# Kernel optimization log

Hardware: AMD Instinct MI355X
Metric: run time of the kernel (lower is better)

Reference implementation:

```python
import jax, jax.numpy as jnp
import numpy as np

EMBED_DIM = 512
KDIM = 64
VDIM = 64


def setup_inputs() -> dict:
    key = jax.random.key(0)
    kx, kq, kk, kv = jax.random.split(key, 4)
    B, S = 4, 4096
    x = jax.random.normal(kx, (B, S, EMBED_DIM), dtype=jnp.float32)
    # nn.Linear(embed_dim, out) weight has shape [out, embed_dim]
    WQ = jax.random.normal(kq, (KDIM, EMBED_DIM), dtype=jnp.float32) * (EMBED_DIM ** -0.5)
    WK = jax.random.normal(kk, (KDIM, EMBED_DIM), dtype=jnp.float32) * (EMBED_DIM ** -0.5)
    WV = jax.random.normal(kv, (VDIM, EMBED_DIM), dtype=jnp.float32) * (EMBED_DIM ** -0.5)
    return {"x": x, "WQ": WQ, "WK": WK, "WV": WV}


def reference(x, WQ, WK, WV):
    # q,k: [B,S,kdim]; v: [B,S,vdim] (self-attention: x[0] is x[-1])
    q = jnp.einsum('bse,ke->bsk', x, WQ)
    k = jnp.einsum('bse,ke->bsk', x, WK)
    v = jnp.einsum('bse,ve->bsv', x, WV)
    scale = k.shape[-1] ** -0.5
    scores = jnp.einsum('bqk,bsk->bqs', q, k) * scale  # [B,S,S]
    # dropout p=0.0 -> identity; masked branch in source is a no-op (non-in-place masked_fill discarded)
    attn = jax.nn.softmax(scores, axis=-1)
    out = jnp.einsum('bqs,bsv->bqv', attn, v)  # [B,S,vdim]
    return out
```

## Files before the change

### kernel.cpp

```cpp
#include <hip/hip_runtime.h>

#define BATCH 4
#define SEQ   4096
#define EMB   512
#define HD    64

typedef __attribute__((ext_vector_type(8))) short short8;
typedef __attribute__((ext_vector_type(4))) float floatx4;

static __device__ __forceinline__ unsigned short f2bf(float f) {
  unsigned u = __builtin_bit_cast(unsigned, f);
  u += 0x7fffu + ((u >> 16) & 1u);
  return (unsigned short)(u >> 16);
}
static __device__ __forceinline__ float bf2f(unsigned short h) {
  unsigned u = ((unsigned)h) << 16;
  return __builtin_bit_cast(float, u);
}
static __device__ __forceinline__ unsigned pack_hi16(float lo, float hi) {
#if __has_builtin(__builtin_amdgcn_perm)
  return __builtin_amdgcn_perm(__builtin_bit_cast(unsigned, hi),
                               __builtin_bit_cast(unsigned, lo), 0x07060302u);
#else
  return (__builtin_bit_cast(unsigned, lo) >> 16) |
         (__builtin_bit_cast(unsigned, hi) & 0xffff0000u);
#endif
}
static __device__ __forceinline__ unsigned pack_f16(float a, float b) {
#if __has_builtin(__builtin_amdgcn_cvt_pkrtz)
  typedef __fp16 fp16v2 __attribute__((ext_vector_type(2)));
  fp16v2 h = __builtin_amdgcn_cvt_pkrtz(a, b);
  return __builtin_bit_cast(unsigned, h);
#else
  _Float16 ha = (_Float16)a, hb = (_Float16)b;
  return (unsigned)__builtin_bit_cast(unsigned short, ha) |
         ((unsigned)__builtin_bit_cast(unsigned short, hb) << 16);
#endif
}
static __device__ __forceinline__ float f16_to_f32(unsigned short bits) {
  _Float16 h = __builtin_bit_cast(_Float16, bits);
  return (float)h;
}

__global__ __launch_bounds__(256) void convw_kernel(
    const float* __restrict__ WQ, const float* __restrict__ WK,
    const float* __restrict__ WV, unsigned short* __restrict__ Wpk)
{
  int t = blockIdx.x * 256 + threadIdx.x;
  int p    = t >> 12;
  int w    = (t >> 10) & 3;
  int kc   = (t >> 6) & 15;
  int lane = t & 63;
  int lr = lane & 15, g = lane >> 4;
  const float* src = (p == 0) ? WQ : ((p == 1) ? WK : WV);
  const float4* s4 = (const float4*)(src + (16 * w + lr) * EMB + kc * 32 + 8 * g);
  float4 a = s4[0], b = s4[1];
  float vv[8] = {a.x, a.y, a.z, a.w, b.x, b.y, b.z, b.w};
  short8 o;
#pragma unroll
  for (int j = 0; j < 8; ++j) {
    unsigned short h = f2bf(vv[j]);
    o[j] = (p == 3) ? (short)f2bf(vv[j] - bf2f(h)) : (short)h;
  }
  *(short8*)(Wpk + (size_t)t * 8) = o;
}

#define XST 40

__global__ __launch_bounds__(256) void proj_kernel(
    const float* __restrict__ x,
    const unsigned short* __restrict__ Wpk,
    unsigned short* __restrict__ Qb,
    unsigned short* __restrict__ Kb,
    unsigned short* __restrict__ VTb)
{
  __shared__ __align__(16) unsigned short Xh[2][32 * XST];
  __shared__ __align__(16) unsigned short Xl[2][32 * XST];

  const int tid  = threadIdx.x;
  const int lane = tid & 63;
  const int w    = tid >> 6;
  const int lr   = lane & 15, g = lane >> 4;
  const long rowBase = (long)blockIdx.x * 32;

  floatx4 accQ[2], accK[2], accV[2];
#pragma unroll
  for (int rt = 0; rt < 2; ++rt) {
    floatx4 z = {0.f, 0.f, 0.f, 0.f};
    accQ[rt] = z; accK[rt] = z; accV[rt] = z;
  }

  const int srow = tid >> 3;
  const int sc   = 4 * (tid & 7);
  const float* xbase = x + (rowBase + srow) * EMB + sc;

  auto stage_write = [&](float4 v, int buf) {
    float vv[4] = {v.x, v.y, v.z, v.w};
    ushort4 hi, lo;
#pragma unroll
    for (int i = 0; i < 4; ++i) {
      unsigned short h = f2bf(vv[i]);
      ((unsigned short*)&hi)[i] = h;
      ((unsigned short*)&lo)[i] = f2bf(vv[i] - bf2f(h));
    }
    *(ushort4*)&Xh[buf][srow * XST + sc] = hi;
    *(ushort4*)&Xl[buf][srow * XST + sc] = lo;
  };

  float4 xv = *(const float4*)(xbase);
  stage_write(xv, 0);
  float4 xnxt = *(const float4*)(xbase + 32);

#pragma unroll 2
  for (int kc = 0; kc < 16; ++kc) {
    __syncthreads();
    const unsigned short* wb = Wpk + (size_t)(w * 16 + kc) * 512 + lane * 8;
    short8 wq  = *(const short8*)(wb);
    short8 wk  = *(const short8*)(wb + 32768);
    short8 wvh = *(const short8*)(wb + 2 * 32768);
    short8 wvl = *(const short8*)(wb + 3 * 32768);
    float4 xfut;
    if (kc + 2 < 16) xfut = *(const float4*)(xbase + (kc + 2) * 32);
    const int buf = kc & 1;
#pragma unroll
    for (int rt = 0; rt < 2; ++rt) {
      short8 xh = *(const short8*)&Xh[buf][(16 * rt + lr) * XST + 8 * g];
      short8 xl = *(const short8*)&Xl[buf][(16 * rt + lr) * XST + 8 * g];
      accQ[rt] = __builtin_amdgcn_mfma_f32_16x16x32_bf16(wq, xh, accQ[rt], 0, 0, 0);
      accK[rt] = __builtin_amdgcn_mfma_f32_16x16x32_bf16(wk, xh, accK[rt], 0, 0, 0);
      accV[rt] = __builtin_amdgcn_mfma_f32_16x16x32_bf16(xh, wvh, accV[rt], 0, 0, 0);
      accV[rt] = __builtin_amdgcn_mfma_f32_16x16x32_bf16(xl, wvh, accV[rt], 0, 0, 0);
      accV[rt] = __builtin_amdgcn_mfma_f32_16x16x32_bf16(xh, wvl, accV[rt], 0, 0, 0);
    }
    if (kc + 1 < 16) { stage_write(xnxt, (kc + 1) & 1); xnxt = xfut; }
  }

  const int bb  = (int)(rowBase >> 12);
  const int sIn = (int)(rowBase & 4095);
#pragma unroll
  for (int rt = 0; rt < 2; ++rt) {
    {
      long row = rowBase + 16 * rt + lr;
      int  col = 16 * w + 4 * g;
      ushort4 u; u.x = f2bf(accQ[rt][0]); u.y = f2bf(accQ[rt][1]);
      u.z = f2bf(accQ[rt][2]); u.w = f2bf(accQ[rt][3]);
      *(ushort4*)(Qb + row * HD + col) = u;
      ushort4 v; v.x = f2bf(accK[rt][0]); v.y = f2bf(accK[rt][1]);
      v.z = f2bf(accK[rt][2]); v.w = f2bf(accK[rt][3]);
      *(ushort4*)(Kb + row * HD + col) = v;
    }
    {
      long addr = ((long)(bb * 64 + 16 * w + lr)) * SEQ + sIn + 16 * rt + 4 * g;
      ushort4 u; u.x = f2bf(accV[rt][0]); u.y = f2bf(accV[rt][1]);
      u.z = f2bf(accV[rt][2]); u.w = f2bf(accV[rt][3]);
      *(ushort4*)(VTb + addr) = u;
    }
  }
}

#define PST 72

__global__ __launch_bounds__(256, 2) void flash_kernel(
    const unsigned short* __restrict__ Qb,
    const unsigned short* __restrict__ Kb,
    const unsigned short* __restrict__ VTb,
    unsigned short* __restrict__ Opart,
    float* __restrict__ Lpart)
{
  __shared__ __align__(16) unsigned short K0lds[64 * 64];
  __shared__ __align__(16) unsigned short V0lds[64 * 64];
  __shared__ __align__(16) unsigned short K1lds[64 * 64];
  __shared__ __align__(16) unsigned short V1lds[64 * 64];
  __shared__ __align__(16) unsigned short Plds[4][64 * PST];

  const int tid  = threadIdx.x;
  const int lane = tid & 63;
  const int w    = tid >> 6;
  const int lr   = lane & 15, g = lane >> 4;
  const int qb   = blockIdx.x >> 3;
  const int ks   = blockIdx.x & 7;
  const int bb   = qb >> 4;
  const long qrow0 = (long)qb * 256 + 64 * w;
  const int  kbase = ks * 512;

  const int koff0 = lr * 64 + 8 * ((    g) ^ (lr & 7));
  const int koff1 = lr * 64 + 8 * ((4 + g) ^ (lr & 7));
  const int voff0 = koff0, voff1 = koff1;
  const int pwoff = lr * PST + 4 * g;
  const int proff = lr * PST + 8 * g;
  unsigned short* const pw = &Plds[w][0];

  const int ci0  = tid;
  const int row0 = ci0 >> 3,        cc0 = (ci0 & 7) ^ (row0 & 7);
  const int ci1  = 256 + tid;
  const int row1 = ci1 >> 3,        cc1 = (ci1 & 7) ^ (row1 & 7);
  const unsigned short* const gK0 = Kb  + ((long)bb * SEQ + kbase + row0) * HD + cc0 * 8;
  const unsigned short* const gK1 = Kb  + ((long)bb * SEQ + kbase + row1) * HD + cc1 * 8;
  const unsigned short* const gV0 = VTb + ((long)bb * HD + row0) * SEQ + kbase + cc0 * 8;
  const unsigned short* const gV1 = VTb + ((long)bb * HD + row1) * SEQ + kbase + cc1 * 8;

  short8 qf[4][2];
#pragma unroll
  for (int qh = 0; qh < 4; ++qh)
#pragma unroll
    for (int ec = 0; ec < 2; ++ec)
      qf[qh][ec] = *(const short8*)(Qb + (qrow0 + 16 * qh + lr) * HD + ec * 32 + 8 * g);

  short8 onesb;
#pragma unroll
  for (int j = 0; j < 8; ++j) onesb[j] = (short)0x3F80;

  floatx4 accO[4][4], accL[4];
#pragma unroll
  for (int qh = 0; qh < 4; ++qh) {
    floatx4 z = {0.f,0.f,0.f,0.f};
    accL[qh] = z;
#pragma unroll
    for (int t = 0; t < 4; ++t) accO[qh][t] = z;
  }
  const float cp = 0.18033688011112042f;
  const float SH = 2.0f;

#define STAGE(kt_, KL, VL) do {                                               \
    const int ko_ = (kt_) * 64;                                               \
    __builtin_amdgcn_global_load_lds(                                         \
        (const __attribute__((address_space(1))) void*)(gK0 + (long)ko_ * HD),\
        (__attribute__((address_space(3))) void*)((KL) + ci0 * 8), 16, 0, 0); \
    __builtin_amdgcn_global_load_lds(                                         \
        (const __attribute__((address_space(1))) void*)(gV0 + ko_),           \
        (__attribute__((address_space(3))) void*)((VL) + ci0 * 8), 16, 0, 0); \
    __builtin_amdgcn_global_load_lds(                                         \
        (const __attribute__((address_space(1))) void*)(gK1 + (long)ko_ * HD),\
        (__attribute__((address_space(3))) void*)((KL) + ci1 * 8), 16, 0, 0); \
    __builtin_amdgcn_global_load_lds(                                         \
        (const __attribute__((address_space(1))) void*)(gV1 + ko_),           \
        (__attribute__((address_space(3))) void*)((VL) + ci1 * 8), 16, 0, 0); \
  } while (0)

#define COMPUTE(KL, VL) do {                                                  \
    short8 kf[2][4];                                                          \
    _Pragma("unroll")                                                         \
    for (int t = 0; t < 4; ++t) {                                             \
      kf[0][t] = *(const short8*)((KL) + koff0 + t * 1024);                   \
      kf[1][t] = *(const short8*)((KL) + koff1 + t * 1024);                   \
    }                                                                         \
    _Pragma("unroll")                                                         \
    for (int qh = 0; qh < 4; ++qh) {                                          \
      floatx4 s_[4];                                                          \
      _Pragma("unroll")                                                       \
      for (int t = 0; t < 4; ++t) { floatx4 z = {0.f,0.f,0.f,0.f}; s_[t] = z; } \
      _Pragma("unroll")                                                       \
      for (int ec = 0; ec < 2; ++ec)                                          \
        _Pragma("unroll")                                                     \
        for (int t = 0; t < 4; ++t)                                           \
          s_[t] = __builtin_amdgcn_mfma_f32_16x16x32_bf16(kf[ec][t], qf[qh][ec], s_[t], 0, 0, 0); \
      _Pragma("unroll")                                                       \
      for (int t = 0; t < 4; ++t) {                                           \
        float p0 = __builtin_amdgcn_exp2f(__builtin_fmaf(s_[t][0], cp, -SH)); \
        float p1 = __builtin_amdgcn_exp2f(__builtin_fmaf(s_[t][1], cp, -SH)); \
        float p2 = __builtin_amdgcn_exp2f(__builtin_fmaf(s_[t][2], cp, -SH)); \
        float p3 = __builtin_amdgcn_exp2f(__builtin_fmaf(s_[t][3], cp, -SH)); \
        uint2 u;                                                              \
        u.x = pack_hi16(p0, p1);                                              \
        u.y = pack_hi16(p2, p3);                                              \
        *(uint2*)(pw + pwoff + qh * (16 * PST) + t * 16) = u;                 \
      }                                                                       \
    }                                                                         \
    short8 vf[2][4];                                                          \
    _Pragma("unroll")                                                         \
    for (int t = 0; t < 4; ++t) {                                             \
      vf[0][t] = *(const short8*)((VL) + voff0 + t * 1024);                   \
      vf[1][t] = *(const short8*)((VL) + voff1 + t * 1024);                   \
    }                                                                         \
    _Pragma("unroll")                                                         \
    for (int qh = 0; qh < 4; ++qh)                                            \
      _Pragma("unroll")                                                       \
      for (int c = 0; c < 2; ++c) {                                           \
        short8 pf = *(const short8*)(pw + proff + qh * (16 * PST) + c * 32);  \
        accL[qh] = __builtin_amdgcn_mfma_f32_16x16x32_bf16(onesb, pf, accL[qh], 0, 0, 0); \
        _Pragma("unroll")                                                     \
        for (int t = 0; t < 4; ++t)                                           \
          accO[qh][t] = __builtin_amdgcn_mfma_f32_16x16x32_bf16(vf[c][t], pf, accO[qh][t], 0, 0, 0); \
      }                                                                       \
  } while (0)

  STAGE(0, K0lds, V0lds);
  for (int kt = 0; kt < 8; kt += 2) {
    __syncthreads();
    STAGE(kt + 1, K1lds, V1lds);
    COMPUTE(K0lds, V0lds);
    __syncthreads();
    if (kt + 2 < 8) STAGE(kt + 2, K0lds, V0lds);
    COMPUTE(K1lds, V1lds);
  }
#undef STAGE
#undef COMPUTE

  unsigned short* obase = Opart + (size_t)(qb * 8 + ks) * 256 * HD;
#pragma unroll
  for (int qh = 0; qh < 4; ++qh) {
    int qlocal = 64 * w + 16 * qh + lr;
#pragma unroll
    for (int t = 0; t < 4; ++t) {
      uint2 u;
      u.x = pack_f16(accO[qh][t][0], accO[qh][t][1]);
      u.y = pack_f16(accO[qh][t][2], accO[qh][t][3]);
      *(uint2*)(obase + qlocal * HD + 16 * t + 4 * g) = u;
    }
    if (g == 0) Lpart[(qb * 8 + ks) * 256 + qlocal] = accL[qh][0];
  }
}

__global__ __launch_bounds__(256) void combine_kernel(
    const unsigned short* __restrict__ Opart, const float* __restrict__ Lpart,
    float* __restrict__ out)
{
  int t   = blockIdx.x * 256 + threadIdx.x;
  int row = t >> 4;
  int d0  = (t & 15) * 4;
  int qb = row >> 8, qi = row & 255;
  float4 acc = {0.f, 0.f, 0.f, 0.f};
  float lt = 0.0f;
#pragma unroll
  for (int ks = 0; ks < 8; ++ks) {
    const unsigned short* p = Opart + ((size_t)(qb * 8 + ks) * 256 + qi) * HD + d0;
    ushort4 v = *(const ushort4*)p;
    acc.x += f16_to_f32(v.x);
    acc.y += f16_to_f32(v.y);
    acc.z += f16_to_f32(v.z);
    acc.w += f16_to_f32(v.w);
    lt += Lpart[(qb * 8 + ks) * 256 + qi];
  }
  float inv = 1.0f / lt;
  float4 o = {acc.x * inv, acc.y * inv, acc.z * inv, acc.w * inv};
  *(float4*)(out + (size_t)row * HD + d0) = o;
}

extern "C" void kernel_launch(void* const* d_in, const int* in_sizes, int n_in,
                              void* d_out, int out_size, void* d_ws, size_t ws_size,
                              hipStream_t stream) {
  const float* x  = (const float*)d_in[0];
  const float* WQ = (const float*)d_in[1];
  const float* WK = (const float*)d_in[2];
  const float* WV = (const float*)d_in[3];

  unsigned short* Qb  = (unsigned short*)d_ws;
  unsigned short* Kb  = Qb  + (size_t)BATCH * SEQ * HD;
  unsigned short* VTb = Kb  + (size_t)BATCH * SEQ * HD;
  unsigned short* Wpk = VTb + (size_t)BATCH * SEQ * HD;
  unsigned short* Opart = Wpk + 262144;
  float* Lpart = (float*)(Opart + (size_t)512 * 256 * HD);

  convw_kernel<<<64, 256, 0, stream>>>(WQ, WK, WV, Wpk);
  proj_kernel<<<(BATCH * SEQ) / 32, 256, 0, stream>>>(x, Wpk, Qb, Kb, VTb);
  flash_kernel<<<512, 256, 0, stream>>>(Qb, Kb, VTb, Opart, Lpart);
  combine_kernel<<<1024, 256, 0, stream>>>(Opart, Lpart, (float*)d_out);
}
```

Baseline: 123.1 us.

## Load x directly from global into MFMA fragments, dropping LDS staging

The projection kernel no longer stages x through double-buffered shared memory with barriers. Each lane now reads its own 8 floats per row tile straight from global memory and splits them into bf16 hi/lo fragments in registers. This removes the LDS writes and reads and the per-iteration __syncthreads. The cost is that all four waves redundantly load and convert the same x data, about four times the global/L2 traffic and conversion work, and there is no longer an explicit prefetch.

```diff
diff --git a/kernel.cpp b/kernel.cpp
--- a/kernel.cpp
+++ b/kernel.cpp
@@ -65,8 +65,6 @@
   *(short8*)(Wpk + (size_t)t * 8) = o;
 }
 
-#define XST 40
-
 __global__ __launch_bounds__(256) void proj_kernel(
     const float* __restrict__ x,
     const unsigned short* __restrict__ Wpk,
@@ -74,15 +72,17 @@
     unsigned short* __restrict__ Kb,
     unsigned short* __restrict__ VTb)
 {
-  __shared__ __align__(16) unsigned short Xh[2][32 * XST];
-  __shared__ __align__(16) unsigned short Xl[2][32 * XST];
-
   const int tid  = threadIdx.x;
   const int lane = tid & 63;
   const int w    = tid >> 6;
   const int lr   = lane & 15, g = lane >> 4;
   const long rowBase = (long)blockIdx.x * 32;
 
+  const float* xp[2];
+  xp[0] = x + (rowBase + lr) * EMB + 8 * g;
+  xp[1] = x + (rowBase + 16 + lr) * EMB + 8 * g;
+  const unsigned short* const wb0 = Wpk + (size_t)(w * 16) * 512 + lane * 8;
+
   floatx4 accQ[2], accK[2], accV[2];
 #pragma unroll
   for (int rt = 0; rt < 2; ++rt) {
@@ -90,49 +90,31 @@
     accQ[rt] = z; accK[rt] = z; accV[rt] = z;
   }
 
-  const int srow = tid >> 3;
-  const int sc   = 4 * (tid & 7);
-  const float* xbase = x + (rowBase + srow) * EMB + sc;
-
-  auto stage_write = [&](float4 v, int buf) {
-    float vv[4] = {v.x, v.y, v.z, v.w};
-    ushort4 hi, lo;
-#pragma unroll
-    for (int i = 0; i < 4; ++i) {
-      unsigned short h = f2bf(vv[i]);
-      ((unsigned short*)&hi)[i] = h;
-      ((unsigned short*)&lo)[i] = f2bf(vv[i] - bf2f(h));
-    }
-    *(ushort4*)&Xh[buf][srow * XST + sc] = hi;
-    *(ushort4*)&Xl[buf][srow * XST + sc] = lo;
-  };
-
-  float4 xv = *(const float4*)(xbase);
-  stage_write(xv, 0);
-  float4 xnxt = *(const float4*)(xbase + 32);
-
-#pragma unroll 2
+#pragma unroll 4
   for (int kc = 0; kc < 16; ++kc) {
-    __syncthreads();
-    const unsigned short* wb = Wpk + (size_t)(w * 16 + kc) * 512 + lane * 8;
+    const unsigned short* wb = wb0 + kc * 512;
     short8 wq  = *(const short8*)(wb);
     short8 wk  = *(const short8*)(wb + 32768);
     short8 wvh = *(const short8*)(wb + 2 * 32768);
     short8 wvl = *(const short8*)(wb + 3 * 32768);
-    float4 xfut;
-    if (kc + 2 < 16) xfut = *(const float4*)(xbase + (kc + 2) * 32);
-    const int buf = kc & 1;
 #pragma unroll
     for (int rt = 0; rt < 2; ++rt) {
-      short8 xh = *(const short8*)&Xh[buf][(16 * rt + lr) * XST + 8 * g];
-      short8 xl = *(const short8*)&Xl[buf][(16 * rt + lr) * XST + 8 * g];
+      const float4* p = (const float4*)(xp[rt] + kc * 32);
+      float4 a = p[0], b = p[1];
+      float vv[8] = {a.x, a.y, a.z, a.w, b.x, b.y, b.z, b.w};
+      short8 xh, xl;
+#pragma unroll
+      for (int i = 0; i < 8; ++i) {
+        unsigned short h = f2bf(vv[i]);
+        xh[i] = (short)h;
+        xl[i] = (short)f2bf(vv[i] - bf2f(h));
+      }
       accQ[rt] = __builtin_amdgcn_mfma_f32_16x16x32_bf16(wq, xh, accQ[rt], 0, 0, 0);
       accK[rt] = __builtin_amdgcn_mfma_f32_16x16x32_bf16(wk, xh, accK[rt], 0, 0, 0);
       accV[rt] = __builtin_amdgcn_mfma_f32_16x16x32_bf16(xh, wvh, accV[rt], 0, 0, 0);
       accV[rt] = __builtin_amdgcn_mfma_f32_16x16x32_bf16(xl, wvh, accV[rt], 0, 0, 0);
       accV[rt] = __builtin_amdgcn_mfma_f32_16x16x32_bf16(xh, wvl, accV[rt], 0, 0, 0);
     }
-    if (kc + 1 < 16) { stage_write(xnxt, (kc + 1) & 1); xnxt = xfut; }
   }
 
   const int bb  = (int)(rowBase >> 12);
```

After: 125.5 us. No clear change (+1.9%).
